# Kernel tuning notes

Measured on AMD Instinct MI355X. Metric: run time of the kernel, lower is better.

Reference implementation:

```python
import jax, jax.numpy as jnp
import numpy as np

N_NODES = 100000
N_EDGES = 500000
E_DIM = 128  # embedding_channels
OUT_DIM = 1


def setup_inputs() -> dict:
    key = jax.random.key(0)
    k_z, k_ei, k_w1, k_w2 = jax.random.split(key, 4)
    z = jax.random.normal(k_z, (N_NODES, E_DIM), dtype=jnp.float32)
    edge_label_index = jax.random.randint(k_ei, (2, N_EDGES), 0, N_NODES, dtype=jnp.int64)
    # MLP([2E, E, out]) params, kaiming-ish scale
    W1 = jax.random.normal(k_w1, (2 * E_DIM, E_DIM), dtype=jnp.float32) * (2.0 / (2 * E_DIM)) ** 0.5
    b1 = jnp.zeros((E_DIM,), dtype=jnp.float32)
    W2 = jax.random.normal(k_w2, (E_DIM, OUT_DIM), dtype=jnp.float32) * (2.0 / E_DIM) ** 0.5
    b2 = jnpp = jnp.zeros((OUT_DIM,), dtype=jnp.float32)
    return {"z": z, "edge_label_index": edge_label_index,
            "W1": W1, "b1": b1, "W2": W2, "b2": b2}


def reference(z, edge_label_index, W1, b1, W2, b2):
    # gather endpoint embeddings and concat: [n_edges, 2E]
    src = z[edge_label_index[0]]  # [n_edges, E]
    dst = z[edge_label_index[1]]  # [n_edges, E]
    x = jnp.concatenate([src, dst], axis=-1)
    # MLP: Linear(2E->E) -> ReLU -> Linear(E->out)
    h = jax.nn.relu(x @ W1 + b1)
    return h @ W2 + b2
```

## Files before the change

### kernel.cpp

```cpp
#include <hip/hip_runtime.h>
#include <hip/hip_bf16.h>

#define N_NODES 100000
#define N_EDGES 500000

using bf16x8 = __attribute__((ext_vector_type(8))) __bf16;
using f32x4  = __attribute__((ext_vector_type(4))) float;


__global__ void cvt_w1f_kernel(const float* __restrict__ W1, __bf16* __restrict__ w1f) {
    int t = blockIdx.x * 256 + threadIdx.x;
    int lane = t & 63, frag = t >> 6;
    int kq = frag >> 4, nt = frag & 15;
    int k0 = kq * 32 + (lane >> 4) * 8;
    int n  = nt * 16 + (lane & 15);
    bf16x8 o;
#pragma unroll
    for (int i = 0; i < 8; i++) {
        int k = k0 + i;
        float w = (n < 128) ? W1[k * 128 + n] : W1[(k + 128) * 128 + (n - 128)];
        o[i] = (__bf16)w;
    }
    ((bf16x8*)w1f)[t] = o;
}

__global__ __launch_bounds__(256, 2) void node_gemm_kernel(
    const float* __restrict__ z, const __bf16* __restrict__ w1f,
    __bf16* __restrict__ C)
{
    __shared__ __bf16 sW[64 * 512];
    {
        const uint4* src = (const uint4*)w1f;
        uint4* dst = (uint4*)sW;
#pragma unroll
        for (int i = 0; i < 16; i++)
            dst[threadIdx.x + 256 * i] = src[threadIdx.x + 256 * i];
    }
    __syncthreads();

    const int lane = threadIdx.x & 63;
    const int wave = threadIdx.x >> 6;
    const int l15 = lane & 15, l4 = lane >> 4;
    const int wr = wave >> 1, wc = wave & 1;
    const int rowbase = blockIdx.x * 128 + wr * 64;

    const float* arow[4];
#pragma unroll
    for (int mt = 0; mt < 4; mt++) {
        int r = rowbase + mt * 16 + l15;
        if (r >= N_NODES) r = N_NODES - 1;
        arow[mt] = z + (size_t)r * 128 + l4 * 8;
    }

    const f32x4 zero = {0.f, 0.f, 0.f, 0.f};
    f32x4 acc[4][8];
#pragma unroll
    for (int mt = 0; mt < 4; mt++)
#pragma unroll
        for (int nt = 0; nt < 8; nt++) acc[mt][nt] = zero;

#pragma unroll
    for (int kq = 0; kq < 4; kq++) {
        bf16x8 bfr[8];
#pragma unroll
        for (int nt = 0; nt < 8; nt++) {
            int fid = kq * 16 + wc * 8 + nt;
            bfr[nt] = *(const bf16x8*)&sW[fid * 512 + lane * 8];
        }
#pragma unroll
        for (int mt = 0; mt < 4; mt++) {
            const float4* p = (const float4*)(arow[mt] + kq * 32);
            float4 x0 = p[0], x1 = p[1];
            bf16x8 a;
            a[0] = (__bf16)x0.x; a[1] = (__bf16)x0.y; a[2] = (__bf16)x0.z; a[3] = (__bf16)x0.w;
            a[4] = (__bf16)x1.x; a[5] = (__bf16)x1.y; a[6] = (__bf16)x1.z; a[7] = (__bf16)x1.w;
#pragma unroll
            for (int nt = 0; nt < 8; nt++)
                acc[mt][nt] = __builtin_amdgcn_mfma_f32_16x16x32_bf16(a, bfr[nt], acc[mt][nt], 0, 0, 0);
        }
    }

#pragma unroll
    for (int mt = 0; mt < 4; mt++) {
#pragma unroll
        for (int j = 0; j < 4; j++) {
            int r = rowbase + mt * 16 + l4 * 4 + j;
            if (r < N_NODES) {
#pragma unroll
                for (int nt = 0; nt < 8; nt++)
                    C[(size_t)r * 256 + wc * 128 + nt * 16 + l15] = (__bf16)acc[mt][nt][j];
            }
        }
    }
}

__global__ __launch_bounds__(256, 4) void edge_kernel(
    const __bf16* __restrict__ C, const int* __restrict__ ei,
    const float* __restrict__ b1, const float* __restrict__ W2,
    const float* __restrict__ b2, float* __restrict__ out)
{
    const int lane = threadIdx.x & 63;
    const int wave = threadIdx.x >> 6;
    const int g = lane >> 4, sub = lane & 15;

    const float4* b1p = (const float4*)(b1 + sub * 8);
    const float4* w2p = (const float4*)(W2 + sub * 8);
    float4 bb0 = b1p[0], bb1 = b1p[1];
    float4 ww0 = w2p[0], ww1 = w2p[1];
    float b1v[8] = {bb0.x, bb0.y, bb0.z, bb0.w, bb1.x, bb1.y, bb1.z, bb1.w};
    float w2v[8] = {ww0.x, ww0.y, ww0.z, ww0.w, ww1.x, ww1.y, ww1.z, ww1.w};
    const float bias2 = b2[0];

    const int wid = blockIdx.x * 4 + wave;
    const int nw  = gridDim.x * 4;

    for (long long eb = (long long)wid * 16; eb < N_EDGES; eb += (long long)nw * 16) {
        bf16x8 cu[4], cv[4];
        long long e[4];
#pragma unroll
        for (int q = 0; q < 4; q++) {
            e[q] = eb + q * 4 + g;
            int is = ei[e[q]];
            int id = ei[N_EDGES + e[q]];
            cu[q] = *(const bf16x8*)(C + (size_t)is * 256 + sub * 8);
            cv[q] = *(const bf16x8*)(C + (size_t)id * 256 + 128 + sub * 8);
        }
#pragma unroll
        for (int q = 0; q < 4; q++) {
            float p = 0.f;
#pragma unroll
            for (int i = 0; i < 8; i++) {
                float h = (float)cu[q][i] + (float)cv[q][i] + b1v[i];
                p += fmaxf(h, 0.f) * w2v[i];
            }
            p += __shfl_xor(p, 1, 64);
            p += __shfl_xor(p, 2, 64);
            p += __shfl_xor(p, 4, 64);
            p += __shfl_xor(p, 8, 64);
            if (sub == 0) out[e[q]] = p + bias2;
        }
    }
}

extern "C" void kernel_launch(void* const* d_in, const int* in_sizes, int n_in,
                              void* d_out, int out_size, void* d_ws, size_t ws_size,
                              hipStream_t stream) {
    const float* z  = (const float*)d_in[0];
    const int*   ei = (const int*)d_in[1];
    const float* W1 = (const float*)d_in[2];
    const float* b1 = (const float*)d_in[3];
    const float* W2 = (const float*)d_in[4];
    const float* b2 = (const float*)d_in[5];
    float* out = (float*)d_out;

    __bf16* w1f = (__bf16*)d_ws;
    __bf16* Cbuf = (__bf16*)((char*)d_ws + 65536);

    cvt_w1f_kernel<<<16, 256, 0, stream>>>(W1, w1f);
    node_gemm_kernel<<<(N_NODES + 127) / 128, 256, 0, stream>>>(z, w1f, Cbuf);
    edge_kernel<<<2048, 256, 0, stream>>>(Cbuf, ei, b1, W2, b2, out);
}
```

Measured before the change: 154.4 us.

## Split node GEMM by output half and store C with permuted vectorized columns

The node GEMM now uses a 2D grid where blockIdx.y selects the src or dst half of W1, so each block stages only half the weights in LDS and each wave computes 64 rows across all 128 columns of that half. The output columns are permuted so each lane writes a contiguous 16-byte bf16x8 vector instead of eight scalar 2-byte stores. The edge kernel reads b1 and W2 with the matching strided permutation, switches to 32-bit edge indices, and raises the occupancy hint. Each block now reads z rows twice (once per half) and the fp32 A operand is loaded and converted per half, which adds z traffic in exchange for coalesced C writes and smaller LDS.

```diff
diff --git a/kernel.cpp b/kernel.cpp
--- a/kernel.cpp
+++ b/kernel.cpp
@@ -11,9 +11,9 @@
 __global__ void cvt_w1f_kernel(const float* __restrict__ W1, __bf16* __restrict__ w1f) {
     int t = blockIdx.x * 256 + threadIdx.x;
     int lane = t & 63, frag = t >> 6;
-    int kq = frag >> 4, nt = frag & 15;
+    int kq = frag >> 4, c16 = frag & 15;
     int k0 = kq * 32 + (lane >> 4) * 8;
-    int n  = nt * 16 + (lane & 15);
+    int n  = c16 * 16 + (lane & 15);
     bf16x8 o;
 #pragma unroll
     for (int i = 0; i < 8; i++) {
@@ -28,21 +28,25 @@
     const float* __restrict__ z, const __bf16* __restrict__ w1f,
     __bf16* __restrict__ C)
 {
-    __shared__ __bf16 sW[64 * 512];
+    __shared__ __bf16 sW[32 * 512];
+    const int h = blockIdx.y;
     {
         const uint4* src = (const uint4*)w1f;
         uint4* dst = (uint4*)sW;
 #pragma unroll
-        for (int i = 0; i < 16; i++)
-            dst[threadIdx.x + 256 * i] = src[threadIdx.x + 256 * i];
+        for (int i = 0; i < 8; i++) {
+            int u = threadIdx.x + 256 * i;
+            int s = u >> 6, w = u & 63;
+            int kq = s >> 3, nt = s & 7;
+            dst[u] = src[(kq * 16 + h * 8 + nt) * 64 + w];
+        }
     }
     __syncthreads();
 
     const int lane = threadIdx.x & 63;
     const int wave = threadIdx.x >> 6;
     const int l15 = lane & 15, l4 = lane >> 4;
-    const int wr = wave >> 1, wc = wave & 1;
-    const int rowbase = blockIdx.x * 128 + wr * 64;
+    const int rowbase = blockIdx.x * 256 + wave * 64;
 
     const float* arow[4];
 #pragma unroll
@@ -63,10 +67,8 @@
     for (int kq = 0; kq < 4; kq++) {
         bf16x8 bfr[8];
 #pragma unroll
-        for (int nt = 0; nt < 8; nt++) {
-            int fid = kq * 16 + wc * 8 + nt;
-            bfr[nt] = *(const bf16x8*)&sW[fid * 512 + lane * 8];
-        }
+        for (int nt = 0; nt < 8; nt++)
+            bfr[nt] = *(const bf16x8*)&sW[(kq * 8 + nt) * 512 + lane * 8];
 #pragma unroll
         for (int mt = 0; mt < 4; mt++) {
             const float4* p = (const float4*)(arow[mt] + kq * 32);
@@ -86,15 +88,16 @@
         for (int j = 0; j < 4; j++) {
             int r = rowbase + mt * 16 + l4 * 4 + j;
             if (r < N_NODES) {
+                bf16x8 o;
 #pragma unroll
-                for (int nt = 0; nt < 8; nt++)
-                    C[(size_t)r * 256 + wc * 128 + nt * 16 + l15] = (__bf16)acc[mt][nt][j];
+                for (int nt = 0; nt < 8; nt++) o[nt] = (__bf16)acc[mt][nt][j];
+                *(bf16x8*)(C + (size_t)r * 256 + h * 128 + l15 * 8) = o;
             }
         }
     }
 }
 
-__global__ __launch_bounds__(256, 4) void edge_kernel(
+__global__ __launch_bounds__(256, 6) void edge_kernel(
     const __bf16* __restrict__ C, const int* __restrict__ ei,
     const float* __restrict__ b1, const float* __restrict__ W2,
     const float* __restrict__ b2, float* __restrict__ out)
@@ -103,20 +106,20 @@
     const int wave = threadIdx.x >> 6;
     const int g = lane >> 4, sub = lane & 15;
 
-    const float4* b1p = (const float4*)(b1 + sub * 8);
-    const float4* w2p = (const float4*)(W2 + sub * 8);
-    float4 bb0 = b1p[0], bb1 = b1p[1];
-    float4 ww0 = w2p[0], ww1 = w2p[1];
-    float b1v[8] = {bb0.x, bb0.y, bb0.z, bb0.w, bb1.x, bb1.y, bb1.z, bb1.w};
-    float w2v[8] = {ww0.x, ww0.y, ww0.z, ww0.w, ww1.x, ww1.y, ww1.z, ww1.w};
+    float b1v[8], w2v[8];
+#pragma unroll
+    for (int i = 0; i < 8; i++) {
+        b1v[i] = b1[i * 16 + sub];
+        w2v[i] = W2[i * 16 + sub];
+    }
     const float bias2 = b2[0];
 
     const int wid = blockIdx.x * 4 + wave;
     const int nw  = gridDim.x * 4;
 
-    for (long long eb = (long long)wid * 16; eb < N_EDGES; eb += (long long)nw * 16) {
+    for (int eb = wid * 16; eb < N_EDGES; eb += nw * 16) {
         bf16x8 cu[4], cv[4];
-        long long e[4];
+        int e[4];
 #pragma unroll
         for (int q = 0; q < 4; q++) {
             e[q] = eb + q * 4 + g;
@@ -130,8 +133,8 @@
             float p = 0.f;
 #pragma unroll
             for (int i = 0; i < 8; i++) {
-                float h = (float)cu[q][i] + (float)cv[q][i] + b1v[i];
-                p += fmaxf(h, 0.f) * w2v[i];
+                float hc = (float)cu[q][i] + (float)cv[q][i] + b1v[i];
+                p += fmaxf(hc, 0.f) * w2v[i];
             }
             p += __shfl_xor(p, 1, 64);
             p += __shfl_xor(p, 2, 64);
@@ -153,10 +156,11 @@
     const float* b2 = (const float*)d_in[5];
     float* out = (float*)d_out;
 
-    __bf16* w1f = (__bf16*)d_ws;
+    __bf16* w1f  = (__bf16*)d_ws;
     __bf16* Cbuf = (__bf16*)((char*)d_ws + 65536);
 
     cvt_w1f_kernel<<<16, 256, 0, stream>>>(W1, w1f);
-    node_gemm_kernel<<<(N_NODES + 127) / 128, 256, 0, stream>>>(z, w1f, Cbuf);
+    dim3 ggrid((N_NODES + 255) / 256, 2);
+    node_gemm_kernel<<<ggrid, 256, 0, stream>>>(z, w1f, Cbuf);
     edge_kernel<<<2048, 256, 0, stream>>>(Cbuf, ei, b1, W2, b2, out);
 }
```

Result: faster. 149.7 us (-3.0%).
